# Kernel tuning notes

Measured on AMD Instinct MI355X. Metric: run time of the kernel, lower is better.

Reference implementation:

```python
import jax, jax.numpy as jnp
import numpy as np


def _gcn_layer(x, row, col, W, b):
    # x: [N, d_in]; row/col: [E'] (with self loops already appended)
    N = x.shape[0]
    deg = jax.ops.segment_sum(jnp.ones_like(row, dtype=x.dtype), row, num_segments=N)
    deg_inv_sqrt = deg ** -0.5  # self loops guarantee deg >= 1
    norm = deg_inv_sqrt[row] * deg_inv_sqrt[col]  # [E']
    msg = norm[:, None] * x[row]                  # gather + normalize
    aggr = jax.ops.segment_sum(msg, col, num_segments=N)  # scatter-add
    return aggr @ W + b


def reference(x, edge_index, W1, b1, W2, b2):
    N = x.shape[0]
    loops = jnp.arange(N, dtype=edge_index.dtype)
    row = jnp.concatenate([edge_index[0], loops])
    col = jnp.concatenate([edge_index[1], loops])
    h = jax.nn.relu(_gcn_layer(x, row, col, W1, b1))
    # F.dropout(training=self.training) is identity in eval mode
    out = _gcn_layer(h, row, col, W2, b2)
    return jax.nn.log_softmax(out, axis=1)


def setup_inputs() -> dict:
    key = jax.random.key(0)
    k1, k2, k3, k4 = jax.random.split(key, 4)
    N, E, F_IN, F_HID, F_OUT = 100000, 1200000, 64, 64, 16
    x = jax.random.normal(k1, (N, F_IN), dtype=jnp.float32)
    edge_index = jax.random.randint(k2, (2, E), 0, N, dtype=jnp.int64)
    W1 = jax.random.normal(k3, (F_IN, F_HID), dtype=jnp.float32) / np.sqrt(F_IN)
    b1 = jnp.zeros((F_HID,), dtype=jnp.float32)
    W2 = jax.random.normal(k4, (F_HID, F_OUT), dtype=jnp.float32) / np.sqrt(F_HID)
    b2 = jnp.zeros((F_OUT,), dtype=jnp.float32)
    return {"x": x, "edge_index": edge_index, "W1": W1, "b1": b1, "W2": W2, "b2": b2}
```

## Files before the change

kernel.cpp:

```cpp
#include <hip/hip_runtime.h>
#include <hip/hip_bf16.h>

typedef __attribute__((ext_vector_type(8))) _Float16 hfrag;
typedef __attribute__((ext_vector_type(4))) float ffrag;
typedef __attribute__((ext_vector_type(4))) _Float16 h4v;

#define BSH 8
#define LBS 256
#define CAP_SH 14
#define CAP (1 << CAP_SH)
#define NF 1024
#define OPAD 520
#define CONV_BLKS 384

__device__ __forceinline__ float b2f_(unsigned short u) {
    return __uint_as_float(((unsigned)u) << 16);
}
__device__ __forceinline__ unsigned short f2b_(float v) {
    __hip_bfloat16 h = __float2bfloat16(v);
    return *reinterpret_cast<unsigned short*>(&h);
}
__device__ __forceinline__ unsigned short f2h_(float v) {
    _Float16 h = (_Float16)v;
    return __builtin_bit_cast(unsigned short, h);
}
__device__ __forceinline__ float h2f_(unsigned short u) {
    _Float16 h = __builtin_bit_cast(_Float16, u);
    return (float)h;
}

__device__ __forceinline__ float loadF(const void* p, long long i, int isF32) {
    if (isF32) return ((const float*)p)[i];
    return b2f_(((const unsigned short*)p)[i]);
}

__device__ __forceinline__ float4 loadF4(const void* p, long long base, int i4, int isF32) {
    if (isF32) {
        return ((const float4*)((const float*)p + base))[i4];
    } else {
        ushort4 u = ((const ushort4*)((const unsigned short*)p + base))[i4];
        return make_float4(b2f_(u.x), b2f_(u.y), b2f_(u.z), b2f_(u.w));
    }
}

__device__ __forceinline__ void get_edge(const int* ei, int i64, int e, int E, int& s, int& d) {
    if (i64) { s = ei[2 * (long long)e]; d = ei[2 * (long long)E + 2 * (long long)e]; }
    else     { s = ei[e];                d = ei[(long long)E + e]; }
}

struct E4 { int s[4]; int d[4]; };
__device__ __forceinline__ E4 load4(const int* __restrict__ ei, int i64, int e0, int E) {
    E4 r;
    if (i64) {
        const int4* ps = (const int4*)(ei + 2 * (long long)e0);
        const int4* pd = (const int4*)(ei + 2 * (long long)E + 2 * (long long)e0);
        int4 a = ps[0], b = ps[1];
        int4 c = pd[0], d = pd[1];
        r.s[0] = a.x; r.s[1] = a.z; r.s[2] = b.x; r.s[3] = b.z;
        r.d[0] = c.x; r.d[1] = c.z; r.d[2] = d.x; r.d[3] = d.z;
    } else {
        int4 a = *(const int4*)(ei + e0);
        int4 c = *(const int4*)(ei + (long long)E + e0);
        r.s[0] = a.x; r.s[1] = a.y; r.s[2] = a.z; r.s[3] = a.w;
        r.d[0] = c.x; r.d[1] = c.y; r.d[2] = c.z; r.d[3] = c.w;
    }
    return r;
}

__device__ __forceinline__ void wave_scan_excl(int* a, int nEl, int lane) {
    int run = 0;
    for (int base = 0; base < nEl; base += 64) {
        int i = base + lane;
        int orig = (i < nEl) ? a[i] : 0;
        int v = orig;
#pragma unroll
        for (int off = 1; off < 64; off <<= 1) {
            int u = __shfl_up(v, off);
            if (lane >= off) v += u;
        }
        if (i < nEl) a[i] = v - orig + run;
        run += __shfl(v, 63);
    }
}

__global__ __launch_bounds__(256) void k_stage(const void* __restrict__ x,
                                               const int* __restrict__ ei,
                                               const void* __restrict__ W1, const void* __restrict__ b1,
                                               const void* __restrict__ W2, const void* __restrict__ b2,
                                               int E, int N, int nbk, int EPB,
                                               int* __restrict__ flags, float* __restrict__ Wbuf,
                                               unsigned short* __restrict__ Wh1,
                                               unsigned short* __restrict__ Wh2,
                                               int* __restrict__ off_d, int* __restrict__ off_s,
                                               int* __restrict__ pdst,
                                               unsigned char* __restrict__ psrc,
                                               unsigned short* __restrict__ xh) {
    __shared__ int hd[512], hs[512], cd[512], cs[512];
    __shared__ int s_sane, s_zero;
    int tid = threadIdx.x;
    if (tid == 0) { s_sane = 0; s_zero = 0; }
    __syncthreads();
    const unsigned short* xu = (const unsigned short*)x;
    if (blockIdx.x == NF) {
        int sane = 0;
        for (int k = tid; k < 4096; k += 256) {
            float v = b2f_(xu[2 * k]);
            float a = fabsf(v);
            if (v == 0.0f || (a >= 9.3e-10f && a <= 1.1e9f)) sane++;
        }
        if (sane) atomicAdd(&s_sane, sane);
        int zero = 0;
        for (int k = tid; k < 1024; k += 256) if (ei[2 * k + 1] == 0) zero++;
        if (zero) atomicAdd(&s_zero, zero);
        __syncthreads();
        int f = (s_sane < 3000) ? 1 : 0;
        if (tid == 0) { flags[0] = f; flags[1] = (s_zero > 512) ? 1 : 0; }
        for (int i = tid; i < 4096; i += 256) Wbuf[i] = loadF(W1, i, f);
        if (tid < 64) Wbuf[4096 + tid] = loadF(b1, tid, f);
        for (int i = tid; i < 1024; i += 256) Wbuf[4160 + i] = loadF(W2, i, f);
        if (tid < 16) Wbuf[5184 + tid] = loadF(b2, tid, f);
        __syncthreads();
        for (int i = tid; i < 4096; i += 256) {
            int j = i & 7, m = (i >> 3) & 15, q = (i >> 7) & 3, kn = i >> 9;
            int kt = kn & 1, nt = kn >> 1;
            Wh1[i] = f2h_(Wbuf[(kt * 32 + q * 8 + j) * 64 + nt * 16 + m]);
        }
        for (int i = tid; i < 1024; i += 256) {
            int j = i & 7, m = (i >> 3) & 15, q = (i >> 7) & 3, kt = i >> 9;
            Wh2[i] = f2h_(Wbuf[4160 + (kt * 32 + q * 8 + j) * 16 + m]);
        }
        return;
    }
    if (blockIdx.x > NF) {
        int cb = blockIdx.x - NF - 1;
        int sane = 0;
        for (int k = tid; k < 4096; k += 256) {
            float v = b2f_(xu[2 * k]);
            float a = fabsf(v);
            if (v == 0.0f || (a >= 9.3e-10f && a <= 1.1e9f)) sane++;
        }
        if (sane) atomicAdd(&s_sane, sane);
        __syncthreads();
        int f = (s_sane < 3000) ? 1 : 0;
        int n4 = N * 16;
        int ctid = cb * 256 + tid;
        int stride = CONV_BLKS * 256 * 2;
        for (int i0 = ctid * 2; i0 < n4; i0 += stride) {
            float4 v0 = loadF4(x, 0, i0, f);
            float4 v1 = (i0 + 1 < n4) ? loadF4(x, 0, i0 + 1, f) : make_float4(0, 0, 0, 0);
            ushort4 o0, o1;
            o0.x = f2h_(v0.x); o0.y = f2h_(v0.y); o0.z = f2h_(v0.z); o0.w = f2h_(v0.w);
            o1.x = f2h_(v1.x); o1.y = f2h_(v1.y); o1.z = f2h_(v1.z); o1.w = f2h_(v1.w);
            ((ushort4*)xh)[i0] = o0;
            if (i0 + 1 < n4) ((ushort4*)xh)[i0 + 1] = o1;
        }
        return;
    }
    int zero = 0;
    for (int k = tid; k < 1024; k += 256) if (ei[2 * k + 1] == 0) zero++;
    if (zero) atomicAdd(&s_zero, zero);
    for (int i = tid; i < 512; i += 256) { hd[i] = 0; hs[i] = 0; }
    __syncthreads();
    int i64 = (s_zero > 512) ? 1 : 0;
    int fb = blockIdx.x;
    int elo = fb * EPB;
    int ehi = min(elo + EPB, E);
    if (elo >= E) {
        for (int b = tid; b <= nbk; b += 256) {
            off_d[fb * OPAD + b] = E; off_s[fb * OPAD + b] = E;
        }
        return;
    }
    int ecnt = ehi - elo;
    for (int e0 = elo + tid * 4; e0 + 4 <= ehi; e0 += 1024) {
        E4 a = load4(ei, i64, e0, E);
#pragma unroll
        for (int u = 0; u < 4; ++u) {
            atomicAdd(&hd[a.d[u] >> BSH], 1);
            atomicAdd(&hs[a.s[u] >> BSH], 1);
        }
    }
    int rem = ecnt & 3, ebase = elo + (ecnt & ~3);
    if (tid < rem) {
        int s, d;
        get_edge(ei, i64, ebase + tid, E, s, d);
        atomicAdd(&hd[d >> BSH], 1);
        atomicAdd(&hs[s >> BSH], 1);
    }
    __syncthreads();
    if (tid < 64)       wave_scan_excl(hd, nbk, tid);
    else if (tid < 128) wave_scan_excl(hs, nbk, tid - 64);
    __syncthreads();
    for (int b = tid; b < nbk; b += 256) {
        int od = elo + hd[b], os = elo + hs[b];
        off_d[fb * OPAD + b] = od; cd[b] = od;
        off_s[fb * OPAD + b] = os; cs[b] = os;
    }
    if (tid == 0) { off_d[fb * OPAD + nbk] = elo + ecnt; off_s[fb * OPAD + nbk] = elo + ecnt; }
    __syncthreads();
    for (int e0 = elo + tid * 4; e0 + 4 <= ehi; e0 += 1024) {
        E4 a = load4(ei, i64, e0, E);
#pragma unroll
        for (int u = 0; u < 4; ++u) {
            int p = atomicAdd(&cd[a.d[u] >> BSH], 1);
            pdst[p] = (a.s[u] << BSH) | (a.d[u] & (LBS - 1));
            int q = atomicAdd(&cs[a.s[u] >> BSH], 1);
            psrc[q] = (unsigned char)(a.s[u] & (LBS - 1));
        }
    }
    if (tid < rem) {
        int s, d;
        get_edge(ei, i64, ebase + tid, E, s, d);
        int p = atomicAdd(&cd[d >> BSH], 1);
        pdst[p] = (s << BSH) | (d & (LBS - 1));
        int q = atomicAdd(&cs[s >> BSH], 1);
        psrc[q] = (unsigned char)(s & (LBS - 1));
    }
}

__global__ __launch_bounds__(256) void k_deg(const unsigned char* __restrict__ psrc,
                                             const int* __restrict__ off_s,
                                             float* __restrict__ dis, int N, int nbk) {
    __shared__ int h[LBS];
    int b = blockIdx.x, tid = threadIdx.x;
    h[tid] = 0;
    __syncthreads();
    for (int fb = tid; fb < NF; fb += 256) {
        int o0 = off_s[fb * OPAD + b];
        int o1 = off_s[fb * OPAD + b + 1];
        for (int p = o0; p < o1; ++p) atomicAdd(&h[psrc[p]], 1);
    }
    __syncthreads();
    int node = b * LBS + tid;
    if (node < N) dis[node] = rsqrtf((float)h[tid] + 1.0f);
}

__global__ __launch_bounds__(256) void k_csr(const int* __restrict__ pdst,
                                             const int* __restrict__ off_d,
                                             const float* __restrict__ dis,
                                             int2* __restrict__ row_se,
                                             int2* __restrict__ pke, int N, int nbk) {
    __shared__ int h[LBS], lb[LBS], cur[LBS];
    int b = blockIdx.x, tid = threadIdx.x;
    h[tid] = 0;
    __syncthreads();
    for (int fb = tid; fb < NF; fb += 256) {
        int o0 = off_d[fb * OPAD + b];
        int o1 = off_d[fb * OPAD + b + 1];
        for (int p = o0; p < o1; ++p) atomicAdd(&h[pdst[p] & (LBS - 1)], 1);
    }
    __syncthreads();
    lb[tid] = h[tid];
    __syncthreads();
    if (tid < 64) wave_scan_excl(lb, LBS, tid);
    __syncthreads();
    int beg = b << CAP_SH;
    cur[tid] = lb[tid];
    int node = b * LBS + tid;
    if (node < N) {
        int s0 = min(lb[tid], CAP), s1 = min(lb[tid] + h[tid], CAP);
        row_se[node] = make_int2(beg + s0, beg + s1);
    }
    __syncthreads();
    for (int fb = tid; fb < NF; fb += 256) {
        int o0 = off_d[fb * OPAD + b];
        int o1 = off_d[fb * OPAD + b + 1];
        for (int p = o0; p < o1; ++p) {
            int e = pdst[p];
            int src = e >> BSH, ld = e & (LBS - 1);
            int r = atomicAdd(&cur[ld], 1);
            if (r < CAP) pke[beg + r] = make_int2(src, __float_as_int(dis[src]));
        }
    }
}

__global__ __launch_bounds__(256) void k_aggdense(const unsigned short* __restrict__ xh,
                                                  const float* __restrict__ dis,
                                                  const int2* __restrict__ row_se,
                                                  const int2* __restrict__ pke,
                                                  const unsigned short* __restrict__ Wh1,
                                                  const unsigned short* __restrict__ Wh2,
                                                  const float* __restrict__ Wbuf,
                                                  unsigned short* __restrict__ t2b, int N) {
    __shared__ __align__(16) unsigned short T[16 * 72];
    int tid = threadIdx.x;
    int lane = tid & 63;
    int w = tid >> 6;
    int g = lane >> 4, i4 = lane & 15;
    int ln = w * 4 + g;
    int n = blockIdx.x * 16 + ln;
    int act = (n < N);
    float4 A[4];
#pragma unroll
    for (int u = 0; u < 4; ++u) A[u] = make_float4(0.f, 0.f, 0.f, 0.f);
    float dd = 0.f;
    int beg = 0, end = 0;
    if (act) {
        dd = dis[n];
        int2 se = row_se[n];
        beg = se.x; end = se.y;
        h4v xv = *(const h4v*)(xh + (long long)n * 64 + i4 * 4);
        float ww = dd * dd;
        A[0].x = ww * (float)xv[0]; A[0].y = ww * (float)xv[1];
        A[0].z = ww * (float)xv[2]; A[0].w = ww * (float)xv[3];
    }
    int cnt = end - beg;
    int Tn = (cnt + 3) >> 2;
    int p = beg;
    int2 e[4];
#pragma unroll
    for (int u = 0; u < 4; ++u) e[u] = pke[p + u];
    for (int t = 0; t < Tn; ++t) {
        h4v hv[4];
#pragma unroll
        for (int u = 0; u < 4; ++u) {
            unsigned ex = min((unsigned)e[u].x, (unsigned)(N - 1));
            hv[u] = *(const h4v*)(xh + (long long)ex * 64 + i4 * 4);
        }
        float nv[4];
#pragma unroll
        for (int u = 0; u < 4; ++u) nv[u] = (p + u < end) ? dd * __int_as_float(e[u].y) : 0.f;
#pragma unroll
        for (int u = 0; u < 4; ++u) e[u] = pke[p + 4 + u];
        p += 4;
#pragma unroll
        for (int u = 0; u < 4; ++u) {
            A[u].x += nv[u] * (float)hv[u][0];
            A[u].y += nv[u] * (float)hv[u][1];
            A[u].z += nv[u] * (float)hv[u][2];
            A[u].w += nv[u] * (float)hv[u][3];
        }
    }
    float4 s;
    s.x = A[0].x + A[1].x + A[2].x + A[3].x;
    s.y = A[0].y + A[1].y + A[2].y + A[3].y;
    s.z = A[0].z + A[1].z + A[2].z + A[3].z;
    s.w = A[0].w + A[1].w + A[2].w + A[3].w;
    ushort4 o;
    o.x = f2h_(s.x); o.y = f2h_(s.y); o.z = f2h_(s.z); o.w = f2h_(s.w);
    *(ushort4*)(&T[ln * 72 + i4 * 4]) = o;
    __syncthreads();
    int m = lane & 15, q = lane >> 4;
    const unsigned short* arow = &T[m * 72 + q * 8];
    hfrag A0 = *(const hfrag*)(arow);
    hfrag A1 = *(const hfrag*)(arow + 32);
    int nt = w;
    hfrag B0 = *(const hfrag*)(Wh1 + (((nt * 2 + 0) * 4 + q) * 16 + m) * 8);
    hfrag B1 = *(const hfrag*)(Wh1 + (((nt * 2 + 1) * 4 + q) * 16 + m) * 8);
    ffrag z = {0.f, 0.f, 0.f, 0.f};
    z = __builtin_amdgcn_mfma_f32_16x16x32_f16(A0, B0, z, 0, 0, 0);
    z = __builtin_amdgcn_mfma_f32_16x16x32_f16(A1, B1, z, 0, 0, 0);
    float b1n = Wbuf[4096 + nt * 16 + m];
    __syncthreads();
#pragma unroll
    for (int r = 0; r < 4; ++r) {
        float hv = fmaxf(z[r] + b1n, 0.0f);
        T[(q * 4 + r) * 72 + nt * 16 + m] = f2h_(hv);
    }
    __syncthreads();
    if (w == 0) {
        const unsigned short* hrow = &T[m * 72 + q * 8];
        hfrag H0 = *(const hfrag*)(hrow);
        hfrag H1 = *(const hfrag*)(hrow + 32);
        hfrag C0 = *(const hfrag*)(Wh2 + ((0 * 4 + q) * 16 + m) * 8);
        hfrag C1 = *(const hfrag*)(Wh2 + ((1 * 4 + q) * 16 + m) * 8);
        ffrag t2 = {0.f, 0.f, 0.f, 0.f};
        t2 = __builtin_amdgcn_mfma_f32_16x16x32_f16(H0, C0, t2, 0, 0, 0);
        t2 = __builtin_amdgcn_mfma_f32_16x16x32_f16(H1, C1, t2, 0, 0, 0);
#pragma unroll
        for (int r = 0; r < 4; ++r) {
            int nn = blockIdx.x * 16 + q * 4 + r;
            if (nn < N) t2b[(size_t)nn * 16 + m] = f2h_(t2[r]);
        }
    }
}

__global__ __launch_bounds__(256) void k_l2(const unsigned short* __restrict__ t2b,
                                            const int* __restrict__ flags,
                                            const float* __restrict__ dis,
                                            const int2* __restrict__ row_se,
                                            const int2* __restrict__ pke,
                                            const float* __restrict__ Wbuf,
                                            void* __restrict__ out, int N) {
    int isF32 = flags[0];
    int tid = threadIdx.x, lane = tid & 63;
    int g = lane >> 4, i = lane & 15;
    int n = blockIdx.x * 16 + (tid >> 6) * 4 + g;
    if (n >= N) return;
    float dd = dis[n];
    int2 se = row_se[n];
    int beg = se.x, end = se.y;
    int cnt = end - beg;
    float A[4];
    A[0] = dd * dd * h2f_(t2b[(size_t)n * 16 + i]);
    A[1] = 0.f; A[2] = 0.f; A[3] = 0.f;
    int T = (cnt + 3) >> 2;
    int p = beg;
    int2 e[4];
#pragma unroll
    for (int u = 0; u < 4; ++u) e[u] = pke[p + u];
    for (int t = 0; t < T; ++t) {
        float r[4];
#pragma unroll
        for (int u = 0; u < 4; ++u) {
            unsigned ex = min((unsigned)e[u].x, (unsigned)(N - 1));
            r[u] = h2f_(t2b[(size_t)ex * 16 + i]);
        }
        float nv[4];
#pragma unroll
        for (int u = 0; u < 4; ++u) nv[u] = (p + u < end) ? dd * __int_as_float(e[u].y) : 0.f;
#pragma unroll
        for (int u = 0; u < 4; ++u) e[u] = pke[p + 4 + u];
        p += 4;
#pragma unroll
        for (int u = 0; u < 4; ++u) A[u] += nv[u] * r[u];
    }
    float a0 = A[0] + A[1] + A[2] + A[3];
    float v = a0 + Wbuf[5184 + i];
    float mx = v;
#pragma unroll
    for (int off = 8; off; off >>= 1) mx = fmaxf(mx, __shfl_xor(mx, off, 16));
    float ex = __expf(v - mx);
    float ss = ex;
#pragma unroll
    for (int off = 8; off; off >>= 1) ss += __shfl_xor(ss, off, 16);
    float r = v - mx - logf(ss);
    size_t oi = (size_t)n * 16 + i;
    if (isF32) ((float*)out)[oi] = r;
    else       ((unsigned short*)out)[oi] = f2b_(r);
}

extern "C" void kernel_launch(void* const* d_in, const int* in_sizes, int n_in,
                              void* d_out, int out_size, void* d_ws, size_t ws_size,
                              hipStream_t stream) {
    const void* x  = d_in[0];
    const int*  ei = (const int*)d_in[1];
    const void* W1 = d_in[2];
    const void* b1 = d_in[3];
    const void* W2 = d_in[4];
    const void* b2 = d_in[5];

    const int N = in_sizes[0] / 64;
    const int E = in_sizes[1] / 2;
    const int nbk = (N + LBS - 1) >> BSH;
    const int EPB = (((E + NF - 1) / NF) + 7) & ~7;

    char* p = (char*)d_ws;
#define CARVE(ty, name, bytes) ty name = (ty)p; p += (((size_t)(bytes)) + 63) & ~(size_t)63;
    CARVE(int*,   flags,     16)
    CARVE(float*, Wbuf,      5200 * 4)
    CARVE(unsigned short*, Wh1, 4096 * 2)
    CARVE(unsigned short*, Wh2, 1024 * 2)
    CARVE(float*, dis,       (size_t)N * 4)
    CARVE(int2*,  row_se,    (size_t)N * 8)
    CARVE(int*,   off_d,     (size_t)NF * OPAD * 4)
    CARVE(int*,   off_s,     (size_t)NF * OPAD * 4)
    CARVE(int*,   pdst,      (size_t)NF * EPB * 4)
    CARVE(unsigned char*, psrc, (size_t)NF * EPB)
    CARVE(int2*,  pke,       (((size_t)nbk << CAP_SH) + 64) * 8)
    CARVE(unsigned short*, xh,   (size_t)N * 64 * 2)
    CARVE(unsigned short*, t2b,  (size_t)N * 16 * 2)
#undef CARVE

    k_stage<<<NF + 1 + CONV_BLKS, 256, 0, stream>>>(x, ei, W1, b1, W2, b2,
                                                    E, N, nbk, EPB,
                                                    flags, Wbuf, Wh1, Wh2,
                                                    off_d, off_s, pdst, psrc, xh);
    k_deg<<<nbk, 256, 0, stream>>>(psrc, off_s, dis, N, nbk);
    k_csr<<<nbk, 256, 0, stream>>>(pdst, off_d, dis, row_se, pke, N, nbk);
    k_aggdense<<<(N + 15) / 16, 256, 0, stream>>>(xh, dis, row_se, pke,
                                                  Wh1, Wh2, Wbuf, t2b, N);
    k_l2<<<(N + 15) / 16, 256, 0, stream>>>(t2b, flags, dis, row_se, pke, Wbuf, d_out, N);
}
```

Before: 202.1 us.

## Fuse degree and CSR build kernels, store only source ids in CSR

Merges the degree and CSR-build kernels into one 512-thread kernel per node bucket. This removes a launch and lets the CSR build skip the scattered dis[src] reads. The CSR edge array now holds only 4-byte source indices instead of (src, dis) pairs, halving the edge stream. The cost is that both aggregation kernels now fetch dis[src] with an extra random gather per edge. The aggregation loops are also unrolled from 4 to 8 edges per iteration to keep more loads in flight, at the price of more registers.

Measured after the change: 190.3 us. 5.8% less time.

```diff
diff --git a/kernel.cpp b/kernel.cpp
--- a/kernel.cpp
+++ b/kernel.cpp
@@ -218,58 +218,57 @@
     }
 }
 
-__global__ __launch_bounds__(256) void k_deg(const unsigned char* __restrict__ psrc,
-                                             const int* __restrict__ off_s,
-                                             float* __restrict__ dis, int N, int nbk) {
-    __shared__ int h[LBS];
+__global__ __launch_bounds__(512) void k_degcsr(const unsigned char* __restrict__ psrc,
+                                                const int* __restrict__ pdst,
+                                                const int* __restrict__ off_s,
+                                                const int* __restrict__ off_d,
+                                                float* __restrict__ dis,
+                                                int2* __restrict__ row_se,
+                                                int* __restrict__ psr, int N, int nbk) {
+    __shared__ int h[LBS], lb[LBS], cur[LBS];
     int b = blockIdx.x, tid = threadIdx.x;
-    h[tid] = 0;
-    __syncthreads();
-    for (int fb = tid; fb < NF; fb += 256) {
+    if (tid < LBS) h[tid] = 0;
+    __syncthreads();
+    for (int fb = tid; fb < NF; fb += 512) {
         int o0 = off_s[fb * OPAD + b];
         int o1 = off_s[fb * OPAD + b + 1];
         for (int p = o0; p < o1; ++p) atomicAdd(&h[psrc[p]], 1);
     }
     __syncthreads();
-    int node = b * LBS + tid;
-    if (node < N) dis[node] = rsqrtf((float)h[tid] + 1.0f);
-}
-
-__global__ __launch_bounds__(256) void k_csr(const int* __restrict__ pdst,
-                                             const int* __restrict__ off_d,
-                                             const float* __restrict__ dis,
-                                             int2* __restrict__ row_se,
-                                             int2* __restrict__ pke, int N, int nbk) {
-    __shared__ int h[LBS], lb[LBS], cur[LBS];
-    int b = blockIdx.x, tid = threadIdx.x;
-    h[tid] = 0;
-    __syncthreads();
-    for (int fb = tid; fb < NF; fb += 256) {
+    if (tid < LBS) {
+        int node = b * LBS + tid;
+        if (node < N) dis[node] = rsqrtf((float)h[tid] + 1.0f);
+    }
+    __syncthreads();
+    if (tid < LBS) h[tid] = 0;
+    __syncthreads();
+    for (int fb = tid; fb < NF; fb += 512) {
         int o0 = off_d[fb * OPAD + b];
         int o1 = off_d[fb * OPAD + b + 1];
         for (int p = o0; p < o1; ++p) atomicAdd(&h[pdst[p] & (LBS - 1)], 1);
     }
     __syncthreads();
-    lb[tid] = h[tid];
+    if (tid < LBS) lb[tid] = h[tid];
     __syncthreads();
     if (tid < 64) wave_scan_excl(lb, LBS, tid);
     __syncthreads();
     int beg = b << CAP_SH;
-    cur[tid] = lb[tid];
-    int node = b * LBS + tid;
-    if (node < N) {
-        int s0 = min(lb[tid], CAP), s1 = min(lb[tid] + h[tid], CAP);
-        row_se[node] = make_int2(beg + s0, beg + s1);
-    }
-    __syncthreads();
-    for (int fb = tid; fb < NF; fb += 256) {
+    if (tid < LBS) {
+        cur[tid] = lb[tid];
+        int node = b * LBS + tid;
+        if (node < N) {
+            int s0 = min(lb[tid], CAP), s1 = min(lb[tid] + h[tid], CAP);
+            row_se[node] = make_int2(beg + s0, beg + s1);
+        }
+    }
+    __syncthreads();
+    for (int fb = tid; fb < NF; fb += 512) {
         int o0 = off_d[fb * OPAD + b];
         int o1 = off_d[fb * OPAD + b + 1];
         for (int p = o0; p < o1; ++p) {
             int e = pdst[p];
-            int src = e >> BSH, ld = e & (LBS - 1);
-            int r = atomicAdd(&cur[ld], 1);
-            if (r < CAP) pke[beg + r] = make_int2(src, __float_as_int(dis[src]));
+            int r = atomicAdd(&cur[e & (LBS - 1)], 1);
+            if (r < CAP) psr[beg + r] = e >> BSH;
         }
     }
 }
@@ -277,7 +276,7 @@
 __global__ __launch_bounds__(256) void k_aggdense(const unsigned short* __restrict__ xh,
                                                   const float* __restrict__ dis,
                                                   const int2* __restrict__ row_se,
-                                                  const int2* __restrict__ pke,
+                                                  const int* __restrict__ psr,
                                                   const unsigned short* __restrict__ Wh1,
                                                   const unsigned short* __restrict__ Wh2,
                                                   const float* __restrict__ Wbuf,
@@ -305,30 +304,32 @@
         A[0].z = ww * (float)xv[2]; A[0].w = ww * (float)xv[3];
     }
     int cnt = end - beg;
-    int Tn = (cnt + 3) >> 2;
+    int Tn = (cnt + 7) >> 3;
     int p = beg;
-    int2 e[4];
-#pragma unroll
-    for (int u = 0; u < 4; ++u) e[u] = pke[p + u];
+    int e[8];
+#pragma unroll
+    for (int u = 0; u < 8; ++u) e[u] = psr[p + u];
     for (int t = 0; t < Tn; ++t) {
-        h4v hv[4];
-#pragma unroll
-        for (int u = 0; u < 4; ++u) {
-            unsigned ex = min((unsigned)e[u].x, (unsigned)(N - 1));
+        h4v hv[8];
+        float dv[8];
+#pragma unroll
+        for (int u = 0; u < 8; ++u) {
+            unsigned ex = min((unsigned)e[u], (unsigned)(N - 1));
             hv[u] = *(const h4v*)(xh + (long long)ex * 64 + i4 * 4);
-        }
-        float nv[4];
-#pragma unroll
-        for (int u = 0; u < 4; ++u) nv[u] = (p + u < end) ? dd * __int_as_float(e[u].y) : 0.f;
-#pragma unroll
-        for (int u = 0; u < 4; ++u) e[u] = pke[p + 4 + u];
-        p += 4;
-#pragma unroll
-        for (int u = 0; u < 4; ++u) {
-            A[u].x += nv[u] * (float)hv[u][0];
-            A[u].y += nv[u] * (float)hv[u][1];
-            A[u].z += nv[u] * (float)hv[u][2];
-            A[u].w += nv[u] * (float)hv[u][3];
+            dv[u] = dis[ex];
+        }
+        float nv[8];
+#pragma unroll
+        for (int u = 0; u < 8; ++u) nv[u] = (p + u < end) ? dd * dv[u] : 0.f;
+#pragma unroll
+        for (int u = 0; u < 8; ++u) e[u] = psr[p + 8 + u];
+        p += 8;
+#pragma unroll
+        for (int u = 0; u < 8; ++u) {
+            A[u & 3].x += nv[u] * (float)hv[u][0];
+            A[u & 3].y += nv[u] * (float)hv[u][1];
+            A[u & 3].z += nv[u] * (float)hv[u][2];
+            A[u & 3].w += nv[u] * (float)hv[u][3];
         }
     }
     float4 s;
@@ -379,7 +380,7 @@
                                             const int* __restrict__ flags,
                                             const float* __restrict__ dis,
                                             const int2* __restrict__ row_se,
-                                            const int2* __restrict__ pke,
+                                            const int* __restrict__ psr,
                                             const float* __restrict__ Wbuf,
                                             void* __restrict__ out, int N) {
     int isF32 = flags[0];
@@ -394,26 +395,27 @@
     float A[4];
     A[0] = dd * dd * h2f_(t2b[(size_t)n * 16 + i]);
     A[1] = 0.f; A[2] = 0.f; A[3] = 0.f;
-    int T = (cnt + 3) >> 2;
+    int T = (cnt + 7) >> 3;
     int p = beg;
-    int2 e[4];
-#pragma unroll
-    for (int u = 0; u < 4; ++u) e[u] = pke[p + u];
+    int e[8];
+#pragma unroll
+    for (int u = 0; u < 8; ++u) e[u] = psr[p + u];
     for (int t = 0; t < T; ++t) {
-        float r[4];
-#pragma unroll
-        for (int u = 0; u < 4; ++u) {
-            unsigned ex = min((unsigned)e[u].x, (unsigned)(N - 1));
+        float r[8], dv[8];
+#pragma unroll
+        for (int u = 0; u < 8; ++u) {
+            unsigned ex = min((unsigned)e[u], (unsigned)(N - 1));
             r[u] = h2f_(t2b[(size_t)ex * 16 + i]);
-        }
-        float nv[4];
-#pragma unroll
-        for (int u = 0; u < 4; ++u) nv[u] = (p + u < end) ? dd * __int_as_float(e[u].y) : 0.f;
-#pragma unroll
-        for (int u = 0; u < 4; ++u) e[u] = pke[p + 4 + u];
-        p += 4;
-#pragma unroll
-        for (int u = 0; u < 4; ++u) A[u] += nv[u] * r[u];
+            dv[u] = dis[ex];
+        }
+        float nv[8];
+#pragma unroll
+        for (int u = 0; u < 8; ++u) nv[u] = (p + u < end) ? dd * dv[u] : 0.f;
+#pragma unroll
+        for (int u = 0; u < 8; ++u) e[u] = psr[p + 8 + u];
+        p += 8;
+#pragma unroll
+        for (int u = 0; u < 8; ++u) A[u & 3] += nv[u] * r[u];
     }
     float a0 = A[0] + A[1] + A[2] + A[3];
     float v = a0 + Wbuf[5184 + i];
@@ -457,7 +459,7 @@
     CARVE(int*,   off_s,     (size_t)NF * OPAD * 4)
     CARVE(int*,   pdst,      (size_t)NF * EPB * 4)
     CARVE(unsigned char*, psrc, (size_t)NF * EPB)
-    CARVE(int2*,  pke,       (((size_t)nbk << CAP_SH) + 64) * 8)
+    CARVE(int*,   psr,       (((size_t)nbk << CAP_SH) + 64) * 4)
     CARVE(unsigned short*, xh,   (size_t)N * 64 * 2)
     CARVE(unsigned short*, t2b,  (size_t)N * 16 * 2)
 #undef CARVE
@@ -466,9 +468,8 @@
                                                     E, N, nbk, EPB,
                                                     flags, Wbuf, Wh1, Wh2,
                                                     off_d, off_s, pdst, psrc, xh);
-    k_deg<<<nbk, 256, 0, stream>>>(psrc, off_s, dis, N, nbk);
-    k_csr<<<nbk, 256, 0, stream>>>(pdst, off_d, dis, row_se, pke, N, nbk);
-    k_aggdense<<<(N + 15) / 16, 256, 0, stream>>>(xh, dis, row_se, pke,
+    k_degcsr<<<nbk, 512, 0, stream>>>(psrc, pdst, off_s, off_d, dis, row_se, psr, N, nbk);
+    k_aggdense<<<(N + 15) / 16, 256, 0, stream>>>(xh, dis, row_se, psr,
                                                   Wh1, Wh2, Wbuf, t2b, N);
-    k_l2<<<(N + 15) / 16, 256, 0, stream>>>(t2b, flags, dis, row_se, pke, Wbuf, d_out, N);
-}
+    k_l2<<<(N + 15) / 16, 256, 0, stream>>>(t2b, flags, dis, row_se, psr, Wbuf, d_out, N);
+}
```

## Replace CSR build with per-bucket shared-memory edge lists and LDS atomic aggregation

Applied to the files above, without the earlier changes.

Drops the k_csr kernel and the pke/row_se CSR arrays. Each block now owns a 128-node bucket, gathers its bucketed edges into a shared-memory list, and accumulates neighbour features with LDS float atomics, then applies the dense MFMA transforms per 128-node tile. The second layer does the same with 16-wide features before the log-softmax. This saves one kernel launch and the CSR write/read traffic, at the cost of heavy LDS atomic contention and a fixed ELC cap that silently drops edges when a bucket has more than 2816 of them.

Measured after the change: 777.7 us. 3.85x slower.

```diff
diff --git a/kernel.cpp b/kernel.cpp
--- a/kernel.cpp
+++ b/kernel.cpp
@@ -5,13 +5,12 @@
 typedef __attribute__((ext_vector_type(4))) float ffrag;
 typedef __attribute__((ext_vector_type(4))) _Float16 h4v;
 
-#define BSH 8
-#define LBS 256
-#define CAP_SH 14
-#define CAP (1 << CAP_SH)
+#define BSH 7
+#define LBS 128
 #define NF 1024
-#define OPAD 520
+#define OPAD 800
 #define CONV_BLKS 384
+#define ELC 2816
 
 __device__ __forceinline__ float b2f_(unsigned short u) {
     return __uint_as_float(((unsigned)u) << 16);
@@ -95,7 +94,7 @@
                                                int* __restrict__ pdst,
                                                unsigned char* __restrict__ psrc,
                                                unsigned short* __restrict__ xh) {
-    __shared__ int hd[512], hs[512], cd[512], cs[512];
+    __shared__ int hd[800], hs[800], cd[800], cs[800];
     __shared__ int s_sane, s_zero;
     int tid = threadIdx.x;
     if (tid == 0) { s_sane = 0; s_zero = 0; }
@@ -159,7 +158,7 @@
     int zero = 0;
     for (int k = tid; k < 1024; k += 256) if (ei[2 * k + 1] == 0) zero++;
     if (zero) atomicAdd(&s_zero, zero);
-    for (int i = tid; i < 512; i += 256) { hd[i] = 0; hs[i] = 0; }
+    for (int i = tid; i < 800; i += 256) { hd[i] = 0; hs[i] = 0; }
     __syncthreads();
     int i64 = (s_zero > 512) ? 1 : 0;
     int fb = blockIdx.x;
@@ -223,7 +222,7 @@
                                              float* __restrict__ dis, int N, int nbk) {
     __shared__ int h[LBS];
     int b = blockIdx.x, tid = threadIdx.x;
-    h[tid] = 0;
+    if (tid < LBS) h[tid] = 0;
     __syncthreads();
     for (int fb = tid; fb < NF; fb += 256) {
         int o0 = off_s[fb * OPAD + b];
@@ -231,203 +230,194 @@
         for (int p = o0; p < o1; ++p) atomicAdd(&h[psrc[p]], 1);
     }
     __syncthreads();
-    int node = b * LBS + tid;
-    if (node < N) dis[node] = rsqrtf((float)h[tid] + 1.0f);
-}
-
-__global__ __launch_bounds__(256) void k_csr(const int* __restrict__ pdst,
+    if (tid < LBS) {
+        int node = b * LBS + tid;
+        if (node < N) dis[node] = rsqrtf((float)h[tid] + 1.0f);
+    }
+}
+
+__global__ __launch_bounds__(512) void k_agg(const unsigned short* __restrict__ xh,
+                                             const float* __restrict__ dis,
                                              const int* __restrict__ off_d,
-                                             const float* __restrict__ dis,
-                                             int2* __restrict__ row_se,
-                                             int2* __restrict__ pke, int N, int nbk) {
-    __shared__ int h[LBS], lb[LBS], cur[LBS];
+                                             const int* __restrict__ pdst,
+                                             const unsigned short* __restrict__ Wh1,
+                                             const unsigned short* __restrict__ Wh2,
+                                             const float* __restrict__ Wbuf,
+                                             unsigned short* __restrict__ t2b, int N) {
+    __shared__ int elist[ELC];
+    __shared__ float acc[LBS * 68];
+    __shared__ __align__(16) unsigned short T[LBS * 72];
+    __shared__ int s_cnt;
     int b = blockIdx.x, tid = threadIdx.x;
-    h[tid] = 0;
-    __syncthreads();
-    for (int fb = tid; fb < NF; fb += 256) {
+    if (tid == 0) s_cnt = 0;
+    for (int i = tid; i < LBS * 68; i += 512) acc[i] = 0.f;
+    __syncthreads();
+    for (int fb = tid; fb < NF; fb += 512) {
         int o0 = off_d[fb * OPAD + b];
         int o1 = off_d[fb * OPAD + b + 1];
-        for (int p = o0; p < o1; ++p) atomicAdd(&h[pdst[p] & (LBS - 1)], 1);
-    }
-    __syncthreads();
-    lb[tid] = h[tid];
-    __syncthreads();
-    if (tid < 64) wave_scan_excl(lb, LBS, tid);
-    __syncthreads();
-    int beg = b << CAP_SH;
-    cur[tid] = lb[tid];
-    int node = b * LBS + tid;
-    if (node < N) {
-        int s0 = min(lb[tid], CAP), s1 = min(lb[tid] + h[tid], CAP);
-        row_se[node] = make_int2(beg + s0, beg + s1);
-    }
-    __syncthreads();
-    for (int fb = tid; fb < NF; fb += 256) {
+        int len = o1 - o0;
+        if (len > 0) {
+            int base = atomicAdd(&s_cnt, len);
+            for (int k = 0; k < len; ++k) {
+                int idx = base + k;
+                if (idx < ELC) elist[idx] = pdst[o0 + k];
+            }
+        }
+    }
+    __syncthreads();
+    int cnt = min(s_cnt, ELC);
+    int i4 = tid & 15;
+    for (int idx = (tid >> 4); idx < cnt; idx += 128) {
+        int j1 = idx + 32, j2 = idx + 64, j3 = idx + 96;
+        int e0 = elist[idx];
+        int e1 = elist[j1 < cnt ? j1 : idx];
+        int e2 = elist[j2 < cnt ? j2 : idx];
+        int e3 = elist[j3 < cnt ? j3 : idx];
+        int s0 = e0 >> BSH, s1 = e1 >> BSH, s2 = e2 >> BSH, s3 = e3 >> BSH;
+        h4v v0 = *(const h4v*)(xh + (long long)s0 * 64 + i4 * 4);
+        h4v v1 = *(const h4v*)(xh + (long long)s1 * 64 + i4 * 4);
+        h4v v2 = *(const h4v*)(xh + (long long)s2 * 64 + i4 * 4);
+        h4v v3 = *(const h4v*)(xh + (long long)s3 * 64 + i4 * 4);
+        float w0 = dis[s0], w1 = dis[s1], w2 = dis[s2], w3 = dis[s3];
+        float* a0 = &acc[(e0 & (LBS - 1)) * 68 + i4 * 4];
+        atomicAdd(&a0[0], w0 * (float)v0[0]);
+        atomicAdd(&a0[1], w0 * (float)v0[1]);
+        atomicAdd(&a0[2], w0 * (float)v0[2]);
+        atomicAdd(&a0[3], w0 * (float)v0[3]);
+        if (j1 < cnt) {
+            float* a1 = &acc[(e1 & (LBS - 1)) * 68 + i4 * 4];
+            atomicAdd(&a1[0], w1 * (float)v1[0]);
+            atomicAdd(&a1[1], w1 * (float)v1[1]);
+            atomicAdd(&a1[2], w1 * (float)v1[2]);
+            atomicAdd(&a1[3], w1 * (float)v1[3]);
+        }
+        if (j2 < cnt) {
+            float* a2 = &acc[(e2 & (LBS - 1)) * 68 + i4 * 4];
+            atomicAdd(&a2[0], w2 * (float)v2[0]);
+            atomicAdd(&a2[1], w2 * (float)v2[1]);
+            atomicAdd(&a2[2], w2 * (float)v2[2]);
+            atomicAdd(&a2[3], w2 * (float)v2[3]);
+        }
+        if (j3 < cnt) {
+            float* a3 = &acc[(e3 & (LBS - 1)) * 68 + i4 * 4];
+            atomicAdd(&a3[0], w3 * (float)v3[0]);
+            atomicAdd(&a3[1], w3 * (float)v3[1]);
+            atomicAdd(&a3[2], w3 * (float)v3[2]);
+            atomicAdd(&a3[3], w3 * (float)v3[3]);
+        }
+    }
+    __syncthreads();
+    for (int idx = tid; idx < LBS * 64; idx += 512) {
+        int ln = idx >> 6, f = idx & 63;
+        int n = b * LBS + ln;
+        unsigned short o = 0;
+        if (n < N) {
+            float dd = dis[n];
+            float xv = h2f_(xh[(long long)n * 64 + f]);
+            o = f2h_(dd * (dd * xv + acc[ln * 68 + f]));
+        }
+        T[ln * 72 + f] = o;
+    }
+    __syncthreads();
+    int lane = tid & 63, w = tid >> 6;
+    int m = lane & 15, q = lane >> 4;
+    const unsigned short* arow = &T[(w * 16 + m) * 72 + q * 8];
+    hfrag A0 = *(const hfrag*)(arow);
+    hfrag A1 = *(const hfrag*)(arow + 32);
+    ffrag z[4];
+#pragma unroll
+    for (int nt = 0; nt < 4; ++nt) {
+        hfrag B0 = *(const hfrag*)(Wh1 + (((nt * 2 + 0) * 4 + q) * 16 + m) * 8);
+        hfrag B1 = *(const hfrag*)(Wh1 + (((nt * 2 + 1) * 4 + q) * 16 + m) * 8);
+        ffrag zz = {0.f, 0.f, 0.f, 0.f};
+        zz = __builtin_amdgcn_mfma_f32_16x16x32_f16(A0, B0, zz, 0, 0, 0);
+        zz = __builtin_amdgcn_mfma_f32_16x16x32_f16(A1, B1, zz, 0, 0, 0);
+        z[nt] = zz;
+    }
+#pragma unroll
+    for (int nt = 0; nt < 4; ++nt) {
+        float b1n = Wbuf[4096 + nt * 16 + m];
+#pragma unroll
+        for (int r = 0; r < 4; ++r) {
+            float hv = fmaxf(z[nt][r] + b1n, 0.0f);
+            T[(w * 16 + q * 4 + r) * 72 + nt * 16 + m] = f2h_(hv);
+        }
+    }
+    const unsigned short* hrow = &T[(w * 16 + m) * 72 + q * 8];
+    hfrag H0 = *(const hfrag*)(hrow);
+    hfrag H1 = *(const hfrag*)(hrow + 32);
+    hfrag C0 = *(const hfrag*)(Wh2 + ((0 * 4 + q) * 16 + m) * 8);
+    hfrag C1 = *(const hfrag*)(Wh2 + ((1 * 4 + q) * 16 + m) * 8);
+    ffrag t2 = {0.f, 0.f, 0.f, 0.f};
+    t2 = __builtin_amdgcn_mfma_f32_16x16x32_f16(H0, C0, t2, 0, 0, 0);
+    t2 = __builtin_amdgcn_mfma_f32_16x16x32_f16(H1, C1, t2, 0, 0, 0);
+#pragma unroll
+    for (int r = 0; r < 4; ++r) {
+        int nn = b * LBS + w * 16 + q * 4 + r;
+        if (nn < N) t2b[(size_t)nn * 16 + m] = f2h_(t2[r]);
+    }
+}
+
+__global__ __launch_bounds__(512) void k_l2(const unsigned short* __restrict__ t2b,
+                                            const int* __restrict__ flags,
+                                            const float* __restrict__ dis,
+                                            const int* __restrict__ off_d,
+                                            const int* __restrict__ pdst,
+                                            const float* __restrict__ Wbuf,
+                                            void* __restrict__ out, int N) {
+    __shared__ int elist[ELC];
+    __shared__ float acc[LBS * 17];
+    __shared__ int s_cnt;
+    int b = blockIdx.x, tid = threadIdx.x;
+    if (tid == 0) s_cnt = 0;
+    for (int i = tid; i < LBS * 17; i += 512) acc[i] = 0.f;
+    __syncthreads();
+    for (int fb = tid; fb < NF; fb += 512) {
         int o0 = off_d[fb * OPAD + b];
         int o1 = off_d[fb * OPAD + b + 1];
-        for (int p = o0; p < o1; ++p) {
-            int e = pdst[p];
-            int src = e >> BSH, ld = e & (LBS - 1);
-            int r = atomicAdd(&cur[ld], 1);
-            if (r < CAP) pke[beg + r] = make_int2(src, __float_as_int(dis[src]));
-        }
-    }
-}
-
-__global__ __launch_bounds__(256) void k_aggdense(const unsigned short* __restrict__ xh,
-                                                  const float* __restrict__ dis,
-                                                  const int2* __restrict__ row_se,
-                                                  const int2* __restrict__ pke,
-                                                  const unsigned short* __restrict__ Wh1,
-                                                  const unsigned short* __restrict__ Wh2,
-                                                  const float* __restrict__ Wbuf,
-                                                  unsigned short* __restrict__ t2b, int N) {
-    __shared__ __align__(16) unsigned short T[16 * 72];
-    int tid = threadIdx.x;
-    int lane = tid & 63;
-    int w = tid >> 6;
-    int g = lane >> 4, i4 = lane & 15;
-    int ln = w * 4 + g;
-    int n = blockIdx.x * 16 + ln;
-    int act = (n < N);
-    float4 A[4];
-#pragma unroll
-    for (int u = 0; u < 4; ++u) A[u] = make_float4(0.f, 0.f, 0.f, 0.f);
-    float dd = 0.f;
-    int beg = 0, end = 0;
-    if (act) {
-        dd = dis[n];
-        int2 se = row_se[n];
-        beg = se.x; end = se.y;
-        h4v xv = *(const h4v*)(xh + (long long)n * 64 + i4 * 4);
-        float ww = dd * dd;
-        A[0].x = ww * (float)xv[0]; A[0].y = ww * (float)xv[1];
-        A[0].z = ww * (float)xv[2]; A[0].w = ww * (float)xv[3];
-    }
-    int cnt = end - beg;
-    int Tn = (cnt + 3) >> 2;
-    int p = beg;
-    int2 e[4];
-#pragma unroll
-    for (int u = 0; u < 4; ++u) e[u] = pke[p + u];
-    for (int t = 0; t < Tn; ++t) {
-        h4v hv[4];
-#pragma unroll
-        for (int u = 0; u < 4; ++u) {
-            unsigned ex = min((unsigned)e[u].x, (unsigned)(N - 1));
-            hv[u] = *(const h4v*)(xh + (long long)ex * 64 + i4 * 4);
-        }
-        float nv[4];
-#pragma unroll
-        for (int u = 0; u < 4; ++u) nv[u] = (p + u < end) ? dd * __int_as_float(e[u].y) : 0.f;
-#pragma unroll
-        for (int u = 0; u < 4; ++u) e[u] = pke[p + 4 + u];
-        p += 4;
-#pragma unroll
-        for (int u = 0; u < 4; ++u) {
-            A[u].x += nv[u] * (float)hv[u][0];
-            A[u].y += nv[u] * (float)hv[u][1];
-            A[u].z += nv[u] * (float)hv[u][2];
-            A[u].w += nv[u] * (float)hv[u][3];
-        }
-    }
-    float4 s;
-    s.x = A[0].x + A[1].x + A[2].x + A[3].x;
-    s.y = A[0].y + A[1].y + A[2].y + A[3].y;
-    s.z = A[0].z + A[1].z + A[2].z + A[3].z;
-    s.w = A[0].w + A[1].w + A[2].w + A[3].w;
-    ushort4 o;
-    o.x = f2h_(s.x); o.y = f2h_(s.y); o.z = f2h_(s.z); o.w = f2h_(s.w);
-    *(ushort4*)(&T[ln * 72 + i4 * 4]) = o;
-    __syncthreads();
-    int m = lane & 15, q = lane >> 4;
-    const unsigned short* arow = &T[m * 72 + q * 8];
-    hfrag A0 = *(const hfrag*)(arow);
-    hfrag A1 = *(const hfrag*)(arow + 32);
-    int nt = w;
-    hfrag B0 = *(const hfrag*)(Wh1 + (((nt * 2 + 0) * 4 + q) * 16 + m) * 8);
-    hfrag B1 = *(const hfrag*)(Wh1 + (((nt * 2 + 1) * 4 + q) * 16 + m) * 8);
-    ffrag z = {0.f, 0.f, 0.f, 0.f};
-    z = __builtin_amdgcn_mfma_f32_16x16x32_f16(A0, B0, z, 0, 0, 0);
-    z = __builtin_amdgcn_mfma_f32_16x16x32_f16(A1, B1, z, 0, 0, 0);
-    float b1n = Wbuf[4096 + nt * 16 + m];
-    __syncthreads();
-#pragma unroll
-    for (int r = 0; r < 4; ++r) {
-        float hv = fmaxf(z[r] + b1n, 0.0f);
-        T[(q * 4 + r) * 72 + nt * 16 + m] = f2h_(hv);
-    }
-    __syncthreads();
-    if (w == 0) {
-        const unsigned short* hrow = &T[m * 72 + q * 8];
-        hfrag H0 = *(const hfrag*)(hrow);
-        hfrag H1 = *(const hfrag*)(hrow + 32);
-        hfrag C0 = *(const hfrag*)(Wh2 + ((0 * 4 + q) * 16 + m) * 8);
-        hfrag C1 = *(const hfrag*)(Wh2 + ((1 * 4 + q) * 16 + m) * 8);
-        ffrag t2 = {0.f, 0.f, 0.f, 0.f};
-        t2 = __builtin_amdgcn_mfma_f32_16x16x32_f16(H0, C0, t2, 0, 0, 0);
-        t2 = __builtin_amdgcn_mfma_f32_16x16x32_f16(H1, C1, t2, 0, 0, 0);
-#pragma unroll
-        for (int r = 0; r < 4; ++r) {
-            int nn = blockIdx.x * 16 + q * 4 + r;
-            if (nn < N) t2b[(size_t)nn * 16 + m] = f2h_(t2[r]);
-        }
-    }
-}
-
-__global__ __launch_bounds__(256) void k_l2(const unsigned short* __restrict__ t2b,
-                                            const int* __restrict__ flags,
-                                            const float* __restrict__ dis,
-                                            const int2* __restrict__ row_se,
-                                            const int2* __restrict__ pke,
-                                            const float* __restrict__ Wbuf,
-                                            void* __restrict__ out, int N) {
+        int len = o1 - o0;
+        if (len > 0) {
+            int base = atomicAdd(&s_cnt, len);
+            for (int k = 0; k < len; ++k) {
+                int idx = base + k;
+                if (idx < ELC) elist[idx] = pdst[o0 + k];
+            }
+        }
+    }
+    __syncthreads();
+    int cnt = min(s_cnt, ELC);
+    int i = tid & 15;
+    for (int idx = (tid >> 4); idx < cnt; idx += 64) {
+        int j1 = idx + 32;
+        int e0 = elist[idx];
+        int e1 = elist[j1 < cnt ? j1 : idx];
+        int s0 = e0 >> BSH, s1 = e1 >> BSH;
+        float v0 = h2f_(t2b[(size_t)s0 * 16 + i]);
+        float v1 = h2f_(t2b[(size_t)s1 * 16 + i]);
+        float w0 = dis[s0], w1 = dis[s1];
+        atomicAdd(&acc[(e0 & (LBS - 1)) * 17 + i], w0 * v0);
+        if (j1 < cnt) atomicAdd(&acc[(e1 & (LBS - 1)) * 17 + i], w1 * v1);
+    }
+    __syncthreads();
     int isF32 = flags[0];
-    int tid = threadIdx.x, lane = tid & 63;
-    int g = lane >> 4, i = lane & 15;
-    int n = blockIdx.x * 16 + (tid >> 6) * 4 + g;
-    if (n >= N) return;
-    float dd = dis[n];
-    int2 se = row_se[n];
-    int beg = se.x, end = se.y;
-    int cnt = end - beg;
-    float A[4];
-    A[0] = dd * dd * h2f_(t2b[(size_t)n * 16 + i]);
-    A[1] = 0.f; A[2] = 0.f; A[3] = 0.f;
-    int T = (cnt + 3) >> 2;
-    int p = beg;
-    int2 e[4];
-#pragma unroll
-    for (int u = 0; u < 4; ++u) e[u] = pke[p + u];
-    for (int t = 0; t < T; ++t) {
-        float r[4];
-#pragma unroll
-        for (int u = 0; u < 4; ++u) {
-            unsigned ex = min((unsigned)e[u].x, (unsigned)(N - 1));
-            r[u] = h2f_(t2b[(size_t)ex * 16 + i]);
-        }
-        float nv[4];
-#pragma unroll
-        for (int u = 0; u < 4; ++u) nv[u] = (p + u < end) ? dd * __int_as_float(e[u].y) : 0.f;
-#pragma unroll
-        for (int u = 0; u < 4; ++u) e[u] = pke[p + 4 + u];
-        p += 4;
-#pragma unroll
-        for (int u = 0; u < 4; ++u) A[u] += nv[u] * r[u];
-    }
-    float a0 = A[0] + A[1] + A[2] + A[3];
-    float v = a0 + Wbuf[5184 + i];
-    float mx = v;
-#pragma unroll
-    for (int off = 8; off; off >>= 1) mx = fmaxf(mx, __shfl_xor(mx, off, 16));
-    float ex = __expf(v - mx);
-    float ss = ex;
-#pragma unroll
-    for (int off = 8; off; off >>= 1) ss += __shfl_xor(ss, off, 16);
-    float r = v - mx - logf(ss);
-    size_t oi = (size_t)n * 16 + i;
-    if (isF32) ((float*)out)[oi] = r;
-    else       ((unsigned short*)out)[oi] = f2b_(r);
+    float b2v = Wbuf[5184 + i];
+    for (int ln = (tid >> 4); ln < LBS; ln += 32) {
+        int n = b * LBS + ln;
+        if (n >= N) continue;
+        float dd = dis[n];
+        float v = dd * (dd * h2f_(t2b[(size_t)n * 16 + i]) + acc[ln * 17 + i]) + b2v;
+        float mx = v;
+#pragma unroll
+        for (int off = 8; off; off >>= 1) mx = fmaxf(mx, __shfl_xor(mx, off, 16));
+        float ex = __expf(v - mx);
+        float ss = ex;
+#pragma unroll
+        for (int off = 8; off; off >>= 1) ss += __shfl_xor(ss, off, 16);
+        float r = v - mx - logf(ss);
+        size_t oi = (size_t)n * 16 + i;
+        if (isF32) ((float*)out)[oi] = r;
+        else       ((unsigned short*)out)[oi] = f2b_(r);
+    }
 }
 
 extern "C" void kernel_launch(void* const* d_in, const int* in_sizes, int n_in,
@@ -452,12 +442,10 @@
     CARVE(unsigned short*, Wh1, 4096 * 2)
     CARVE(unsigned short*, Wh2, 1024 * 2)
     CARVE(float*, dis,       (size_t)N * 4)
-    CARVE(int2*,  row_se,    (size_t)N * 8)
     CARVE(int*,   off_d,     (size_t)NF * OPAD * 4)
     CARVE(int*,   off_s,     (size_t)NF * OPAD * 4)
     CARVE(int*,   pdst,      (size_t)NF * EPB * 4)
     CARVE(unsigned char*, psrc, (size_t)NF * EPB)
-    CARVE(int2*,  pke,       (((size_t)nbk << CAP_SH) + 64) * 8)
     CARVE(unsigned short*, xh,   (size_t)N * 64 * 2)
     CARVE(unsigned short*, t2b,  (size_t)N * 16 * 2)
 #undef CARVE
@@ -467,8 +455,6 @@
                                                     flags, Wbuf, Wh1, Wh2,
                                                     off_d, off_s, pdst, psrc, xh);
     k_deg<<<nbk, 256, 0, stream>>>(psrc, off_s, dis, N, nbk);
-    k_csr<<<nbk, 256, 0, stream>>>(pdst, off_d, dis, row_se, pke, N, nbk);
-    k_aggdense<<<(N + 15) / 16, 256, 0, stream>>>(xh, dis, row_se, pke,
-                                                  Wh1, Wh2, Wbuf, t2b, N);
-    k_l2<<<(N + 15) / 16, 256, 0, stream>>>(t2b, flags, dis, row_se, pke, Wbuf, d_out, N);
-}
+    k_agg<<<nbk, 512, 0, stream>>>(xh, dis, off_d, pdst, Wh1, Wh2, Wbuf, t2b, N);
+    k_l2<<<nbk, 512, 0, stream>>>(t2b, flags, dis, off_d, pdst, Wbuf, d_out, N);
+}
```
